# Optimization experiments

Measured on AMD Instinct MI355X. Metric: run time of the kernel, lower is better.

The kernel has to match this reference:

```python
import jax, jax.numpy as jnp
import numpy as np

EPS = 1e-12  # torch F.normalize eps


def setup_inputs() -> dict:
    key = jax.random.key(0)
    k1, k2, k3, k4 = jax.random.split(key, 4)
    B, N, K, C, H = 4, 2304, 8, 512, 8
    X_flat = jax.random.normal(k1, (B, N, C), dtype=jnp.float32)
    S_tokens = jax.random.normal(k2, (B, K, C), dtype=jnp.float32)
    Wqkv = jax.random.normal(k3, (C, 3 * C), dtype=jnp.float32) * (1.0 / np.sqrt(C))
    Wout = jax.random.normal(k4, (C, C), dtype=jnp.float32) * (1.0 / np.sqrt(C))
    temperature = jnp.ones((H, 1, 1), dtype=jnp.float32)
    return {"X_flat": X_flat, "S_tokens": S_tokens, "Wqkv": Wqkv,
            "Wout": Wout, "temperature": temperature}


def _l2norm(x):
    # matches torch.nn.functional.normalize(x, dim=-1)
    n = jnp.linalg.norm(x, axis=-1, keepdims=True)
    return x / jnp.maximum(n, EPS)


def reference(X_flat, S_tokens, Wqkv, Wout, temperature):
    B, N, C = X_flat.shape
    H = temperature.shape[0]
    D = C // H
    X_in = jnp.concatenate([X_flat, S_tokens], axis=1)  # (B, Nt, C)
    Nt = X_in.shape[1]
    qkv = X_in @ Wqkv  # (B, Nt, 3C)
    q, k, v = jnp.split(qkv, 3, axis=-1)
    # (B, H, Nt, D)
    q = q.reshape(B, Nt, H, D).transpose(0, 2, 1, 3)
    k = k.reshape(B, Nt, H, D).transpose(0, 2, 1, 3)
    v = v.reshape(B, Nt, H, D).transpose(0, 2, 1, 3)
    q = _l2norm(q)
    k = _l2norm(k)
    attn = jnp.einsum('bhqd,bhkd->bhqk', q, k) * temperature[None]  # (B,H,Nt,Nt)
    attn = jax.nn.softmax(attn, axis=-1)
    out = jnp.einsum('bhqk,bhkd->bhqd', attn, v)
    out = out.transpose(0, 2, 1, 3).reshape(B, Nt, C)
    out = out @ Wout
    return out[:, :N, :]
```

## Files before the change

### kernel.cpp

```cpp
#include <hip/hip_runtime.h>
#include <math.h>

typedef unsigned short u16;
typedef unsigned int   u32;
typedef __attribute__((ext_vector_type(8)))  __bf16 bf16x8;
typedef __attribute__((ext_vector_type(16))) float  f32x16;

constexpr int Bc  = 4;
constexpr int Nc  = 2304;
constexpr int KSc = 8;
constexpr int Cc  = 512;
constexpr int Hc  = 8;
constexpr int Dc  = 64;
constexpr int NTc = Nc + KSc;
constexpr int M1c = Bc * NTc;
constexpr int N1c = 3 * Cc;
constexpr int M2c = Bc * Nc;
constexpr int QT128 = Nc / 128;
constexpr int KT64  = NTc / 64;
constexpr int NSPL  = 3;
constexpr float LOG2E = 1.4426950408889634f;

__device__ __forceinline__ u32 f2bf1(float f) {
    u32 u = __float_as_uint(f);
    return (u + 0x7fffu + ((u >> 16) & 1u)) >> 16;
}
__device__ __forceinline__ u32 pk2(float lo, float hi) {
    u32 ul = __float_as_uint(lo);
    u32 uh = __float_as_uint(hi);
    ul = (ul + 0x7fffu + ((ul >> 16) & 1u)) >> 16;
    uh = (uh + 0x7fffu + ((uh >> 16) & 1u)) & 0xffff0000u;
    return ul | uh;
}
__device__ __forceinline__ float bf2f(u16 x) {
    return __uint_as_float(((u32)x) << 16);
}
__device__ __forceinline__ u32 pkb(float lo, float hi) {
    union { u32 u; __bf16 h[2]; } t;
    t.h[0] = (__bf16)lo; t.h[1] = (__bf16)hi;
    return t.u;
}
__device__ __forceinline__ void gll16(const u16* g, char* l) {
    __builtin_amdgcn_global_load_lds(
        (const __attribute__((address_space(1))) unsigned int*)g,
        (__attribute__((address_space(3))) unsigned int*)l, 16, 0, 0);
}

#define MFMA32(A, B, C) __builtin_amdgcn_mfma_f32_32x32x16_bf16(A, B, C, 0, 0, 0)

union U4 { u32 u[4]; bf16x8 f; };

__global__ __launch_bounds__(256)
void cvt_concat(const float* __restrict__ X, const float* __restrict__ S,
                u16* __restrict__ A)
{
    const int id  = blockIdx.x * 256 + threadIdx.x;
    const int row = id >> 6;
    const int ch  = (id & 63) * 8;
    const int b = row / NTc, t = row - b * NTc;
    const float* src = (t < Nc) ? X + ((size_t)(b * Nc + t)) * Cc + ch
                                : S + ((size_t)(b * KSc + (t - Nc))) * Cc + ch;
    const float4 v0 = ((const float4*)src)[0];
    const float4 v1 = ((const float4*)src)[1];
    u32 w[4];
    w[0] = pk2(v0.x, v0.y); w[1] = pk2(v0.z, v0.w);
    w[2] = pk2(v1.x, v1.y); w[3] = pk2(v1.z, v1.w);
    *(uint4*)(A + (size_t)row * Cc + ch) = *(const uint4*)w;
}

__global__ __launch_bounds__(256)
void cvt_w2(const float* __restrict__ Wqkv, const float* __restrict__ Wout,
            u16* __restrict__ WqT, u16* __restrict__ WoT)
{
    __shared__ float Ws[64][68];
    const bool second = (blockIdx.x >= N1c / 64);
    const float* W = second ? Wout : Wqkv;
    u16*        WT = second ? WoT  : WqT;
    const int   Nn = second ? Cc   : N1c;
    const int n0 = (second ? (blockIdx.x - N1c / 64) : blockIdx.x) * 64;
    const int k0 = blockIdx.y * 64;
#pragma unroll
    for (int i = 0; i < 4; ++i) {
        const int c = i * 256 + threadIdx.x;
        const int kr = c >> 4, nc = (c & 15) * 4;
        const float4 v = *(const float4*)(W + (size_t)(k0 + kr) * Nn + n0 + nc);
        Ws[kr][nc] = v.x; Ws[kr][nc+1] = v.y; Ws[kr][nc+2] = v.z; Ws[kr][nc+3] = v.w;
    }
    __syncthreads();
#pragma unroll
    for (int i = 0; i < 2; ++i) {
        const int c = i * 256 + threadIdx.x;
        const int n = c >> 3, kc = (c & 7) * 8;
        u32 wh[4];
#pragma unroll
        for (int j = 0; j < 4; ++j)
            wh[j] = pk2(Ws[kc + 2*j][n], Ws[kc + 2*j + 1][n]);
        *(uint4*)(WT + (size_t)(n0 + n) * Cc + k0 + kc) = *(const uint4*)wh;
    }
}

__global__ __launch_bounds__(256)
void gemm_qkv(const u16* __restrict__ A, const u16* __restrict__ Bw,
              const float* __restrict__ temp,
              u16* __restrict__ Qb, u16* __restrict__ Kb, u16* __restrict__ Vt)
{
    __shared__ __align__(16) u16 lds[2 * 2 * 8192];
    char* L = (char*)lds;

    const int tid = threadIdx.x;
    const int wid = tid >> 6, lane = tid & 63, hi = lane >> 5, ln = lane & 31;
    const int wm = wid >> 1, wn = wid & 1;
    const int m0 = blockIdx.x * 128, n0 = blockIdx.y * 128;

    const int sr = tid >> 3;
    const int sc = tid & 7;

    f32x16 acc[2][2];
#pragma unroll
    for (int i = 0; i < 2; ++i)
#pragma unroll
        for (int j = 0; j < 2; ++j)
#pragma unroll
            for (int r = 0; r < 16; ++r) acc[i][j][r] = 0.f;

#define QKV_STAGE(BUF, K0)                                                     \
    do {                                                                       \
        char* dA = L + (BUF) * 32768;                                          \
        char* dB = dA + 16384;                                                 \
        _Pragma("unroll")                                                      \
        for (int i_ = 0; i_ < 4; ++i_) {                                       \
            const int row_ = i_ * 32 + sr;                                     \
            const int gc_  = (sc ^ (row_ & 7)) * 8;                            \
            int mg_ = m0 + row_; if (mg_ > M1c - 1) mg_ = M1c - 1;             \
            gll16(A  + (size_t)mg_ * Cc + (K0) + gc_,                          \
                  dA + i_ * 4096 + tid * 16);                                  \
            gll16(Bw + (size_t)(n0 + row_) * Cc + (K0) + gc_,                  \
                  dB + i_ * 4096 + tid * 16);                                  \
        }                                                                      \
    } while (0)

    QKV_STAGE(0, 0);
    __syncthreads();

    for (int k0 = 0; k0 < Cc; k0 += 64) {
        const int cur = (k0 >> 6) & 1;
        if (k0 + 64 < Cc) QKV_STAGE(cur ^ 1, k0 + 64);
        const char* ldsA = L + cur * 32768;
        const char* ldsB = ldsA + 16384;
#pragma unroll
        for (int ks = 0; ks < 4; ++ks) {
            bf16x8 af[2], bfr[2];
#pragma unroll
            for (int f = 0; f < 2; ++f) {
                const int mr = wm * 64 + f * 32 + ln;
                af[f]  = *(const bf16x8*)(ldsA + mr * 128 + (((ks * 2 + hi) ^ (mr & 7)) << 4));
                const int nr = wn * 64 + f * 32 + ln;
                bfr[f] = *(const bf16x8*)(ldsB + nr * 128 + (((ks * 2 + hi) ^ (nr & 7)) << 4));
            }
#pragma unroll
            for (int fm = 0; fm < 2; ++fm)
#pragma unroll
                for (int fn = 0; fn < 2; ++fn)
                    acc[fm][fn] = MFMA32(af[fm], bfr[fn], acc[fm][fn]);
        }
        __syncthreads();
    }
#undef QKV_STAGE

    const int which = n0 >> 9;
    const int hh = ((n0 + wn * 64) >> 6) & 7;

    if (which < 2) {
        const float tsc = (which == 0) ? temp[hh] : LOG2E;
#pragma unroll
        for (int fm = 0; fm < 2; ++fm)
#pragma unroll
            for (int r = 0; r < 16; ++r) {
                float ss = fmaf(acc[fm][0][r], acc[fm][0][r],
                                acc[fm][1][r] * acc[fm][1][r]);
                ss += __shfl_xor(ss, 1);
                ss += __shfl_xor(ss, 2);
                ss += __shfl_xor(ss, 4);
                ss += __shfl_xor(ss, 8);
                ss += __shfl_xor(ss, 16);
                const float scl = tsc / fmaxf(sqrtf(ss), 1e-12f);
                acc[fm][0][r] *= scl;
                acc[fm][1][r] *= scl;
            }

#pragma unroll
        for (int fm = 0; fm < 2; ++fm)
#pragma unroll
            for (int fn = 0; fn < 2; ++fn) {
                const int ng = n0 + wn * 64 + fn * 32 + ln;
                const int h = (ng >> 6) & 7, d = ng & 63;
                u16* base = (which == 0) ? Qb : Kb;
#pragma unroll
                for (int r = 0; r < 16; ++r) {
                    const int mg = m0 + wm * 64 + fm * 32 + (r & 3) + 8 * (r >> 2) + 4 * hi;
                    if (mg < M1c) {
                        const int b = mg / NTc, t = mg - b * NTc;
                        base[((size_t)((b * Hc + h) * NTc + t)) * Dc + d] = (u16)f2bf1(acc[fm][fn][r]);
                    }
                }
            }
    } else {
#pragma unroll
        for (int fm = 0; fm < 2; ++fm)
#pragma unroll
            for (int fn = 0; fn < 2; ++fn) {
                const int ng = n0 + wn * 64 + fn * 32 + ln;
                const int h = (ng >> 6) & 7, d = ng & 63;
#pragma unroll
                for (int g = 0; g < 4; ++g) {
                    const int mg = m0 + wm * 64 + fm * 32 + 8 * g + 4 * hi;
                    if (mg < M1c) {
                        const int b = mg / NTc, t = mg - b * NTc;
                        uint2 v;
                        v.x = f2bf1(acc[fm][fn][4*g])   | (f2bf1(acc[fm][fn][4*g+1]) << 16);
                        v.y = f2bf1(acc[fm][fn][4*g+2]) | (f2bf1(acc[fm][fn][4*g+3]) << 16);
                        *(uint2*)(Vt + ((size_t)((b * Hc + h) * Dc + d)) * NTc + t) = v;
                    }
                }
            }
    }
}

__global__ __launch_bounds__(256)
void gemm_out(const u16* __restrict__ Ahg, const u16* __restrict__ Bhg,
              float* __restrict__ Out)
{
    __shared__ __align__(16) u16 lds[2 * 6144];
    char* L = (char*)lds;

    const int tid = threadIdx.x;
    const int wid = tid >> 6, lane = tid & 63, hi = lane >> 5, ln = lane & 31;
    const int wm = wid >> 1, wn = wid & 1;
    const int m0 = blockIdx.x * 128, n0 = blockIdx.y * 64;
    const int sr2 = tid >> 2;
    const int sc2 = tid & 3;

    f32x16 acc[2];
#pragma unroll
    for (int i = 0; i < 2; ++i)
#pragma unroll
        for (int r = 0; r < 16; ++r) acc[i][r] = 0.f;

#define OUT_STAGE(BUF, K0)                                                     \
    do {                                                                       \
        char* bb = L + (BUF) * 12288;                                          \
        _Pragma("unroll")                                                      \
        for (int i_ = 0; i_ < 2; ++i_) {                                       \
            const int row_ = i_ * 64 + sr2;                                    \
            const int gc_  = (sc2 ^ (row_ & 3)) * 8;                           \
            const size_t go_ = (size_t)(m0 + row_) * Cc + (K0) + gc_;          \
            gll16(Ahg + go_, bb + i_ * 4096 + tid * 16);                       \
        }                                                                      \
        {                                                                      \
            const int gc_  = (sc2 ^ (sr2 & 3)) * 8;                            \
            const size_t go_ = (size_t)(n0 + sr2) * Cc + (K0) + gc_;           \
            gll16(Bhg + go_, bb + 8192 + tid * 16);                            \
        }                                                                      \
    } while (0)

    OUT_STAGE(0, 0);
    __syncthreads();

    for (int k0 = 0; k0 < Cc; k0 += 32) {
        const int cur = (k0 >> 5) & 1;
        if (k0 + 32 < Cc) OUT_STAGE(cur ^ 1, k0 + 32);
        const char* bb = L + cur * 12288;
        const char* pAh = bb;
        const char* pBh = bb + 8192;
#pragma unroll
        for (int ks = 0; ks < 2; ++ks) {
            bf16x8 afh[2], bfh;
#pragma unroll
            for (int f = 0; f < 2; ++f) {
                const int mr = wm * 64 + f * 32 + ln;
                const int moff = mr * 64 + (((ks * 2 + hi) ^ (mr & 3)) << 4);
                afh[f] = *(const bf16x8*)(pAh + moff);
            }
            {
                const int nr = wn * 32 + ln;
                const int noff = nr * 64 + (((ks * 2 + hi) ^ (nr & 3)) << 4);
                bfh = *(const bf16x8*)(pBh + noff);
            }
#pragma unroll
            for (int fm = 0; fm < 2; ++fm)
                acc[fm] = MFMA32(afh[fm], bfh, acc[fm]);
        }
        __syncthreads();
    }
#undef OUT_STAGE

#pragma unroll
    for (int fm = 0; fm < 2; ++fm) {
        const int ng = n0 + wn * 32 + ln;
#pragma unroll
        for (int r = 0; r < 16; ++r) {
            const int mg = m0 + wm * 64 + fm * 32 + (r & 3) + 8 * (r >> 2) + 4 * hi;
            Out[(size_t)mg * Cc + ng] = acc[fm][r];
        }
    }
}

__global__ __launch_bounds__(256)
void attn_mfma(const u16* __restrict__ Qbf, const u16* __restrict__ Kbf,
               const u16* __restrict__ Vtg, const float* __restrict__ temp,
               float* __restrict__ Op, float* __restrict__ Rs)
{
    __shared__ __align__(16) u16 ldsKV[2][2][4096];
    char* L = (char*)ldsKV;

    const int tid  = threadIdx.x;
    const int wid  = tid >> 6;
    const int lane = tid & 63;
    const int hi   = lane >> 5;
    const int ln   = lane & 31;
    const int blk  = (blockIdx.x & 7) * (Bc * Hc * QT128 * NSPL / 8)
                   + (blockIdx.x >> 3);
    const int sp   = blk % NSPL;
    const int qb   = blk / NSPL;
    const int bh   = qb / QT128;
    const int qt   = qb - bh * QT128;
    const int b    = bh >> 3, h = bh & 7;
    const int qbase = qt * 128 + wid * 32;
    const float mlc = fabsf(temp[h]) * LOG2E;
    const int ktb = (sp == 0) ? 0 : (sp == 1 ? 13 : 26);
    const int kte = (sp == 0) ? 13 : (sp == 1 ? 26 : (KT64 + 1));

    const u16* Qrow = Qbf + ((size_t)bh * NTc + qbase + ln) * Dc;
    bf16x8 qf[4];
#pragma unroll
    for (int ks = 0; ks < 4; ++ks)
        qf[ks] = *(const bf16x8*)(Qrow + ks * 16 + hi * 8);

    U4 ones;
    ones.u[0] = ones.u[1] = ones.u[2] = ones.u[3] = 0x3F803F80u;

    f32x16 o0, o1, rsacc;
#pragma unroll
    for (int r = 0; r < 16; ++r) { o0[r] = 0.f; o1[r] = 0.f; rsacc[r] = 0.f; }

    const u16* Kbh = Kbf + (size_t)bh * NTc * Dc;
    const u16* Vbh = Vtg + (size_t)bh * Dc * NTc;

    const int sc  = tid & 7;
    const int sr0 = tid >> 3;

#define ATTN_STAGE(BUF, KB)                                                    \
    do {                                                                       \
        char* Kd = L + (BUF) * 16384;                                          \
        char* Vd = Kd + 8192;                                                  \
        _Pragma("unroll")                                                      \
        for (int half_ = 0; half_ < 2; ++half_) {                              \
            const int r_ = sr0 + half_ * 32;                                   \
            const int gc_ = (sc ^ (r_ & 7)) * 8;                               \
            int rK = (KB) + r_;   if (rK > NTc - 1) rK = NTc - 1;              \
            int cV = (KB) + gc_;  if (cV > NTc - 8) cV = NTc - 8;              \
            gll16(Kbh + (size_t)rK * Dc + gc_, Kd + half_ * 4096 + tid * 16);  \
            gll16(Vbh + (size_t)r_ * NTc + cV, Vd + half_ * 4096 + tid * 16);  \
        }                                                                      \
    } while (0)

    ATTN_STAGE(0, ktb * 64);
    __syncthreads();

    for (int kt = ktb; kt < kte; ++kt) {
        const int  cur  = (kt - ktb) & 1;
        const bool tail = (kt == KT64);
        if (kt + 1 < kte) ATTN_STAGE(cur ^ 1, (kt + 1) * 64);
        const char* Kc = L + cur * 16384;
        const char* Vc = Kc + 8192;

        const int nsub = tail ? 1 : 2;
        for (int kt2 = 0; kt2 < nsub; ++kt2) {
            f32x16 s;
#pragma unroll
            for (int r = 0; r < 16; ++r) s[r] = 0.f;
            const int krow = kt2 * 32 + ln;
            const char* kbc = Kc + (krow << 7);
            const int   ksz = (krow & 7) << 4;
            __builtin_amdgcn_s_setprio(1);
#pragma unroll
            for (int ks = 0; ks < 4; ++ks) {
                const bf16x8 kf = *(const bf16x8*)(kbc + (((ks << 5) + (hi << 4)) ^ ksz));
                s = MFMA32(kf, qf[ks], s);
            }
            __builtin_amdgcn_s_setprio(0);

            float p[16];
#pragma unroll
            for (int r = 0; r < 16; ++r)
                p[r] = __builtin_amdgcn_exp2f(s[r] - mlc);
            if (tail) {
#pragma unroll
                for (int r = 4; r < 16; ++r) p[r] = 0.f;
            }

            u32 a0 = pkb(p[0],  p[1]),  a1 = pkb(p[2],  p[3]);
            u32 b0 = pkb(p[4],  p[5]),  b1 = pkb(p[6],  p[7]);
            u32 c0 = pkb(p[8],  p[9]),  c1 = pkb(p[10], p[11]);
            u32 d0 = pkb(p[12], p[13]), d1 = pkb(p[14], p[15]);
            asm("v_permlane32_swap_b32 %0, %1" : "+v"(a0), "+v"(b0));
            asm("v_permlane32_swap_b32 %0, %1" : "+v"(a1), "+v"(b1));
            asm("v_permlane32_swap_b32 %0, %1" : "+v"(c0), "+v"(d0));
            asm("v_permlane32_swap_b32 %0, %1" : "+v"(c1), "+v"(d1));
            U4 f0, f1;
            f0.u[0] = a0; f0.u[1] = a1; f0.u[2] = b0; f0.u[3] = b1;
            f1.u[0] = c0; f1.u[1] = c1; f1.u[2] = d0; f1.u[3] = d1;

            const char* v0c = Vc + (ln << 7);
            const char* v1c = Vc + ((32 + ln) << 7);
            const int   vsz0 = (ln & 7) << 4;
            const int   cof0 = ((kt2 << 6) + (hi << 4)) ^ vsz0;
            const int   cof1 = ((kt2 << 6) + 32 + (hi << 4)) ^ vsz0;
            __builtin_amdgcn_s_setprio(1);
            rsacc = MFMA32(ones.f, f0.f, rsacc);
            o0 = MFMA32(*(const bf16x8*)(v0c + cof0), f0.f, o0);
            o1 = MFMA32(*(const bf16x8*)(v1c + cof0), f0.f, o1);
            if (!tail) {
                rsacc = MFMA32(ones.f, f1.f, rsacc);
                o0 = MFMA32(*(const bf16x8*)(v0c + cof1), f1.f, o0);
                o1 = MFMA32(*(const bf16x8*)(v1c + cof1), f1.f, o1);
            }
            __builtin_amdgcn_s_setprio(0);
        }
        __syncthreads();
    }
#undef ATTN_STAGE

    if (hi == 0)
        Rs[((size_t)sp * 32 + bh) * Nc + qbase + ln] = rsacc[0];

    float* Po = Op + (size_t)sp * M2c * Cc
                   + ((size_t)b * Nc + qbase + ln) * Cc + h * Dc;
#pragma unroll
    for (int g = 0; g < 4; ++g) {
        *(float4*)(Po + 8 * g + 4 * hi) =
            make_float4(o0[4*g], o0[4*g+1], o0[4*g+2], o0[4*g+3]);
        *(float4*)(Po + 32 + 8 * g + 4 * hi) =
            make_float4(o1[4*g], o1[4*g+1], o1[4*g+2], o1[4*g+3]);
    }
}

__global__ __launch_bounds__(256)
void merge_o(const float* __restrict__ Op, const float* __restrict__ Rs,
             u16* __restrict__ Oh)
{
    const int id = blockIdx.x * 256 + threadIdx.x;
    const size_t base = (size_t)id * 4;
    const int row = id >> 7;
    const int c   = (int)(base & 511);
    const int b   = row / Nc, qi = row - b * Nc;
    const int bh  = b * Hc + (c >> 6);
    const float rs = Rs[(size_t)bh * Nc + qi]
                   + Rs[(size_t)(32 + bh) * Nc + qi]
                   + Rs[(size_t)(64 + bh) * Nc + qi];
    const float inv = 1.0f / rs;
    const float4 va = *(const float4*)(Op + base);
    const float4 vb = *(const float4*)(Op + (size_t)M2c * Cc + base);
    const float4 vc = *(const float4*)(Op + 2 * (size_t)M2c * Cc + base);
    uint2 hv;
    hv.x = pk2((va.x + vb.x + vc.x) * inv, (va.y + vb.y + vc.y) * inv);
    hv.y = pk2((va.z + vb.z + vc.z) * inv, (va.w + vb.w + vc.w) * inv);
    *(uint2*)(Oh + base) = hv;
}

extern "C" void kernel_launch(void* const* d_in, const int* in_sizes, int n_in,
                              void* d_out, int out_size, void* d_ws, size_t ws_size,
                              hipStream_t stream)
{
    const float* X    = (const float*)d_in[0];
    const float* S    = (const float*)d_in[1];
    const float* Wqkv = (const float*)d_in[2];
    const float* Wout = (const float*)d_in[3];
    const float* temp = (const float*)d_in[4];
    float* out = (float*)d_out;

    u16* ws16 = (u16*)d_ws;
    const size_t R  = (size_t)M1c * Cc;
    const size_t RO = (size_t)M2c * Cc;

    float* Op  = (float*)ws16;
    u16*  Abf  = ws16;
    u16*  WqT  = ws16 + 2 * R;
    u16*  WoT  = ws16 + 6 * RO;
    u16*  Qbf  = WoT + (size_t)Cc * Cc;
    u16*  Kbf  = Qbf + R;
    u16*  Vt   = Kbf + R;
    float* Rs  = (float*)(Vt + R);
    u16*  Oh   = Qbf;

    cvt_concat<<<M1c * (Cc / 8) / 256, 256, 0, stream>>>(X, S, Abf);
    cvt_w2<<<dim3(N1c / 64 + Cc / 64, Cc / 64), 256, 0, stream>>>(Wqkv, Wout, WqT, WoT);
    gemm_qkv<<<dim3((M1c + 127) / 128, N1c / 128), 256, 0, stream>>>(Abf, WqT, temp, Qbf, Kbf, Vt);
    attn_mfma<<<Bc * Hc * QT128 * NSPL, 256, 0, stream>>>(Qbf, Kbf, Vt, temp, Op, Rs);
    merge_o<<<(int)(RO / 4 / 256), 256, 0, stream>>>(Op, Rs, Oh);
    gemm_out<<<dim3(M2c / 128, Cc / 64), 256, 0, stream>>>(Oh, WoT, out);
}
```

Before: 148.0 us.

## Fuse prep conversion kernels, remap gemm_out blocks, seed attention MFMA from zero register

Merges the activation concat/convert kernel and the weight transpose/convert kernel into one launch, removing one kernel launch and its tail. Switches gemm_out to a 1-D grid with an index remap so consecutive blocks are spread across N-columns, which may change L2 and cache locality across the XCDs. In attention, the first QK MFMA now takes a preserved zero vector as its accumulator instead of re-zeroing s on every subtile, saving 16 register moves per iteration.

```diff
diff --git a/kernel.cpp b/kernel.cpp
--- a/kernel.cpp
+++ b/kernel.cpp
@@ -50,35 +50,43 @@
 
 union U4 { u32 u[4]; bf16x8 f; };
 
+constexpr int NCONC = M1c * (Cc / 8) / 256;
+constexpr int NWQ   = (N1c / 64) * (Cc / 64);
+constexpr int NWO   = (Cc / 64) * (Cc / 64);
+
 __global__ __launch_bounds__(256)
-void cvt_concat(const float* __restrict__ X, const float* __restrict__ S,
-                u16* __restrict__ A)
+void prep(const float* __restrict__ X, const float* __restrict__ S,
+          u16* __restrict__ A,
+          const float* __restrict__ Wqkv, const float* __restrict__ Wout,
+          u16* __restrict__ WqT, u16* __restrict__ WoT)
 {
-    const int id  = blockIdx.x * 256 + threadIdx.x;
-    const int row = id >> 6;
-    const int ch  = (id & 63) * 8;
-    const int b = row / NTc, t = row - b * NTc;
-    const float* src = (t < Nc) ? X + ((size_t)(b * Nc + t)) * Cc + ch
-                                : S + ((size_t)(b * KSc + (t - Nc))) * Cc + ch;
-    const float4 v0 = ((const float4*)src)[0];
-    const float4 v1 = ((const float4*)src)[1];
-    u32 w[4];
-    w[0] = pk2(v0.x, v0.y); w[1] = pk2(v0.z, v0.w);
-    w[2] = pk2(v1.x, v1.y); w[3] = pk2(v1.z, v1.w);
-    *(uint4*)(A + (size_t)row * Cc + ch) = *(const uint4*)w;
-}
-
-__global__ __launch_bounds__(256)
-void cvt_w2(const float* __restrict__ Wqkv, const float* __restrict__ Wout,
-            u16* __restrict__ WqT, u16* __restrict__ WoT)
-{
+    const int bid = blockIdx.x;
+    if (bid < NCONC) {
+        const int id  = bid * 256 + threadIdx.x;
+        const int row = id >> 6;
+        const int ch  = (id & 63) * 8;
+        const int b = row / NTc, t = row - b * NTc;
+        const float* src = (t < Nc) ? X + ((size_t)(b * Nc + t)) * Cc + ch
+                                    : S + ((size_t)(b * KSc + (t - Nc))) * Cc + ch;
+        const float4 v0 = ((const float4*)src)[0];
+        const float4 v1 = ((const float4*)src)[1];
+        u32 w[4];
+        w[0] = pk2(v0.x, v0.y); w[1] = pk2(v0.z, v0.w);
+        w[2] = pk2(v1.x, v1.y); w[3] = pk2(v1.z, v1.w);
+        *(uint4*)(A + (size_t)row * Cc + ch) = *(const uint4*)w;
+        return;
+    }
+
     __shared__ float Ws[64][68];
-    const bool second = (blockIdx.x >= N1c / 64);
+    const int widx  = bid - NCONC;
+    const bool second = (widx >= NWQ);
+    const int  lidx = second ? (widx - NWQ) : widx;
     const float* W = second ? Wout : Wqkv;
     u16*        WT = second ? WoT  : WqT;
     const int   Nn = second ? Cc   : N1c;
-    const int n0 = (second ? (blockIdx.x - N1c / 64) : blockIdx.x) * 64;
-    const int k0 = blockIdx.y * 64;
+    const int ncols = Nn / 64;
+    const int n0 = (lidx % ncols) * 64;
+    const int k0 = (lidx / ncols) * 64;
 #pragma unroll
     for (int i = 0; i < 4; ++i) {
         const int c = i * 256 + threadIdx.x;
@@ -236,7 +244,8 @@
     const int tid = threadIdx.x;
     const int wid = tid >> 6, lane = tid & 63, hi = lane >> 5, ln = lane & 31;
     const int wm = wid >> 1, wn = wid & 1;
-    const int m0 = blockIdx.x * 128, n0 = blockIdx.y * 64;
+    const int sem = (blockIdx.x & 7) * 72 + (blockIdx.x >> 3);
+    const int m0 = (sem % 72) * 128, n0 = (sem / 72) * 64;
     const int sr2 = tid >> 2;
     const int sc2 = tid & 3;
 
@@ -339,9 +348,10 @@
     U4 ones;
     ones.u[0] = ones.u[1] = ones.u[2] = ones.u[3] = 0x3F803F80u;
 
-    f32x16 o0, o1, rsacc;
-#pragma unroll
-    for (int r = 0; r < 16; ++r) { o0[r] = 0.f; o1[r] = 0.f; rsacc[r] = 0.f; }
+    f32x16 o0, o1, rsacc, z16;
+#pragma unroll
+    for (int r = 0; r < 16; ++r) { o0[r] = 0.f; o1[r] = 0.f; rsacc[r] = 0.f; z16[r] = 0.f; }
+    asm volatile("" : "+v"(z16));
 
     const u16* Kbh = Kbf + (size_t)bh * NTc * Dc;
     const u16* Vbh = Vtg + (size_t)bh * Dc * NTc;
@@ -376,15 +386,17 @@
 
         const int nsub = tail ? 1 : 2;
         for (int kt2 = 0; kt2 < nsub; ++kt2) {
-            f32x16 s;
-#pragma unroll
-            for (int r = 0; r < 16; ++r) s[r] = 0.f;
             const int krow = kt2 * 32 + ln;
             const char* kbc = Kc + (krow << 7);
             const int   ksz = (krow & 7) << 4;
+            f32x16 s;
             __builtin_amdgcn_s_setprio(1);
-#pragma unroll
-            for (int ks = 0; ks < 4; ++ks) {
+            {
+                const bf16x8 kf0 = *(const bf16x8*)(kbc + (((hi << 4)) ^ ksz));
+                s = MFMA32(kf0, qf[0], z16);
+            }
+#pragma unroll
+            for (int ks = 1; ks < 4; ++ks) {
                 const bf16x8 kf = *(const bf16x8*)(kbc + (((ks << 5) + (hi << 4)) ^ ksz));
                 s = MFMA32(kf, qf[ks], s);
             }
@@ -493,10 +505,9 @@
     float* Rs  = (float*)(Vt + R);
     u16*  Oh   = Qbf;
 
-    cvt_concat<<<M1c * (Cc / 8) / 256, 256, 0, stream>>>(X, S, Abf);
-    cvt_w2<<<dim3(N1c / 64 + Cc / 64, Cc / 64), 256, 0, stream>>>(Wqkv, Wout, WqT, WoT);
+    prep<<<NCONC + NWQ + NWO, 256, 0, stream>>>(X, S, Abf, Wqkv, Wout, WqT, WoT);
     gemm_qkv<<<dim3((M1c + 127) / 128, N1c / 128), 256, 0, stream>>>(Abf, WqT, temp, Qbf, Kbf, Vt);
     attn_mfma<<<Bc * Hc * QT128 * NSPL, 256, 0, stream>>>(Qbf, Kbf, Vt, temp, Op, Rs);
     merge_o<<<(int)(RO / 4 / 256), 256, 0, stream>>>(Op, Rs, Oh);
-    gemm_out<<<dim3(M2c / 128, Cc / 64), 256, 0, stream>>>(Oh, WoT, out);
-}
+    gemm_out<<<576, 256, 0, stream>>>(Oh, WoT, out);
+}
```

After: 151.9 us. 1.03x slower.
